# Kernel optimization log

Measured on AMD Instinct MI355X. Metric: run time of the kernel, lower is better.

Reference implementation:

```python
import jax, jax.numpy as jnp
import numpy as np

# BD feature layout (matches init_kwargs BD dict)
MARK_AX = 0
OP_SHL = 1
OP_SHR = 2
ALU_LO = 16
ALU_HI = 32
AX_CARRY_LO = 48
OUTPUT_LO = 64
OUTPUT_HI = 80
D = 128
B, S = 32, 8192


def setup_inputs() -> dict:
    key = jax.random.key(0)
    x_bd = jax.random.normal(key, (B, S, D), dtype=jnp.float32)
    return {"x_bd": x_bd}


def reference(x_bd):
    # decode operands from one-hot-ish nibble slices  [B, S]
    val_lo = jnp.argmax(x_bd[..., ALU_LO:ALU_LO + 16], axis=-1).astype(jnp.int32)
    val_hi = jnp.argmax(x_bd[..., ALU_HI:ALU_HI + 16], axis=-1).astype(jnp.int32)
    value = val_lo + (val_hi << 4)                                 # 0..255
    shift = jnp.minimum(
        jnp.argmax(x_bd[..., AX_CARRY_LO:AX_CARRY_LO + 16], axis=-1).astype(jnp.int32), 31)

    mark = x_bd[..., MARK_AX] >= 0.5
    shl = x_bd[..., OP_SHL] > 0.5
    shr = x_bd[..., OP_SHR] > 0.5
    active = mark & (shl | shr)

    pow2 = jnp.left_shift(jnp.int32(1), shift)                     # 2**shift, exact
    res_shl = (value * pow2) & 255                                 # SHL mod 256
    res_shr = value // pow2                                        # SHR floor
    result = jnp.where(shl, res_shl, res_shr)

    res_lo = result & 15
    res_hi = (result >> 4) & 15
    # scatter +2.0 into OUTPUT_LO/HI bins via one-hot (vectorized over B*S)
    add = 2.0 * (jax.nn.one_hot(OUTPUT_LO + res_lo, D, dtype=x_bd.dtype)
                 + jax.nn.one_hot(OUTPUT_HI + res_hi, D, dtype=x_bd.dtype))
    return x_bd + jnp.where(active[..., None], add, jnp.zeros((), x_bd.dtype))
```

## Files before the change

kernel.cpp:

```cpp
#include <hip/hip_runtime.h>

#define DD 128

__global__ __launch_bounds__(256) void byteshift_kernel(const float* __restrict__ x,
                                                        float* __restrict__ out,
                                                        int n_rows) {
    int tid = blockIdx.x * blockDim.x + threadIdx.x;
    int lane_r = tid & 31;
    int row = tid >> 5;
    if (row >= n_rows) return;

    const float4* xrow = (const float4*)(x + (size_t)row * DD);
    float4 v = xrow[lane_r];

    int dbase = lane_r * 4;
    float m = v.x; int mi = dbase;
    if (v.y > m) { m = v.y; mi = dbase + 1; }
    if (v.z > m) { m = v.z; mi = dbase + 2; }
    if (v.w > m) { m = v.w; mi = dbase + 3; }

    #pragma unroll
    for (int dlt = 1; dlt <= 2; dlt <<= 1) {
        float om = __shfl_xor(m, dlt);
        int   oi = __shfl_xor(mi, dlt);
        if (om > m || (om == m && oi < mi)) { m = om; mi = oi; }
    }

    int flags = (v.x >= 0.5f ? 1 : 0) | (v.y > 0.5f ? 2 : 0) | (v.z > 0.5f ? 4 : 0);
    flags = __shfl(flags, 0, 32);

    int d_lo = __shfl(mi, 4, 32);
    int d_hi = __shfl(mi, 8, 32);
    int d_sh = __shfl(mi, 12, 32);

    int value = (d_lo & 15) | ((d_hi & 15) << 4);
    int shift = d_sh & 15;
    bool shl    = (flags & 2) != 0;
    bool active = (flags & 1) && (flags & 6);
    int result = shl ? ((value << shift) & 255) : (value >> shift);
    int t0 = 64 + (result & 15);
    int t1 = 80 + ((result >> 4) & 15);

    float add = active ? 2.0f : 0.0f;
    float4 o = v;
    if (dbase     == t0 || dbase     == t1) o.x += add;
    if (dbase + 1 == t0 || dbase + 1 == t1) o.y += add;
    if (dbase + 2 == t0 || dbase + 2 == t1) o.z += add;
    if (dbase + 3 == t0 || dbase + 3 == t1) o.w += add;
    ((float4*)(out + (size_t)row * DD))[lane_r] = o;
}

extern "C" void kernel_launch(void* const* d_in, const int* in_sizes, int n_in,
                              void* d_out, int out_size, void* d_ws, size_t ws_size,
                              hipStream_t stream) {
    const float* x = (const float*)d_in[0];
    float* out = (float*)d_out;
    int n_rows = in_sizes[0] / DD;
    int threads = 256;
    int total = n_rows * 32;
    int blocks = (total + threads - 1) / threads;
    hipLaunchKernelGGL(byteshift_kernel, dim3(blocks), dim3(threads), 0, stream,
                       x, out, n_rows);
}
```

Baseline: 216.1 us.

## Map 8 lanes per row with 16 floats each and nontemporal accesses

Each thread now handles a full 16-wide nibble group (four 16-byte vectors) instead of 4 floats, so the argmax is computed in-thread with no cross-lane reduction shuffles. Rows use 8 lanes, loads and stores use nontemporal builtins, and the +2.0 scatter becomes a single per-lane index compare. This cuts shuffle and ALU work and aims for streaming memory behaviour. The trade-off is fewer threads in flight and each lane touching 64 contiguous bytes rather than the fully coalesced pattern across lanes.

```diff
diff --git a/kernel.cpp b/kernel.cpp
--- a/kernel.cpp
+++ b/kernel.cpp
@@ -1,53 +1,61 @@
 #include <hip/hip_runtime.h>
 
 #define DD 128
+
+typedef float f32x4 __attribute__((ext_vector_type(4)));
 
 __global__ __launch_bounds__(256) void byteshift_kernel(const float* __restrict__ x,
                                                         float* __restrict__ out,
                                                         int n_rows) {
     int tid = blockIdx.x * blockDim.x + threadIdx.x;
-    int lane_r = tid & 31;
-    int row = tid >> 5;
+    int lane = tid & 7;
+    int row = tid >> 3;
     if (row >= n_rows) return;
 
-    const float4* xrow = (const float4*)(x + (size_t)row * DD);
-    float4 v = xrow[lane_r];
+    const f32x4* xr = (const f32x4*)(x + (size_t)row * DD) + lane * 4;
+    f32x4 v0 = __builtin_nontemporal_load(xr + 0);
+    f32x4 v1 = __builtin_nontemporal_load(xr + 1);
+    f32x4 v2 = __builtin_nontemporal_load(xr + 2);
+    f32x4 v3 = __builtin_nontemporal_load(xr + 3);
 
-    int dbase = lane_r * 4;
-    float m = v.x; int mi = dbase;
-    if (v.y > m) { m = v.y; mi = dbase + 1; }
-    if (v.z > m) { m = v.z; mi = dbase + 2; }
-    if (v.w > m) { m = v.w; mi = dbase + 3; }
+    float f[16] = {v0.x, v0.y, v0.z, v0.w, v1.x, v1.y, v1.z, v1.w,
+                   v2.x, v2.y, v2.z, v2.w, v3.x, v3.y, v3.z, v3.w};
+
+    float m = f[0]; int mi = 0;
+    #pragma unroll
+    for (int j = 1; j < 16; ++j)
+        if (f[j] > m) { m = f[j]; mi = j; }
+
+    int flags = (f[0] >= 0.5f ? 1 : 0) | (f[1] > 0.5f ? 2 : 0) | (f[2] > 0.5f ? 4 : 0);
+    flags     = __shfl(flags, 0, 8);
+    int n_lo  = __shfl(mi, 1, 8);
+    int n_hi  = __shfl(mi, 2, 8);
+    int n_sh  = __shfl(mi, 3, 8);
+
+    int value   = n_lo | (n_hi << 4);
+    bool shl    = (flags & 2) != 0;
+    bool active = (flags & 1) && (flags & 6);
+    int result  = shl ? ((value << n_sh) & 255) : (value >> n_sh);
+
+    int t0 = 64 + (result & 15);
+    int t1 = 80 + (result >> 4);
+    int dbase = lane << 4;
+    int tsel  = (dbase == 80) ? t1 : t0;
+    int r     = active ? (tsel - dbase) : -1;
 
     #pragma unroll
-    for (int dlt = 1; dlt <= 2; dlt <<= 1) {
-        float om = __shfl_xor(m, dlt);
-        int   oi = __shfl_xor(mi, dlt);
-        if (om > m || (om == m && oi < mi)) { m = om; mi = oi; }
-    }
+    for (int j = 0; j < 16; ++j)
+        if (r == j) f[j] += 2.0f;
 
-    int flags = (v.x >= 0.5f ? 1 : 0) | (v.y > 0.5f ? 2 : 0) | (v.z > 0.5f ? 4 : 0);
-    flags = __shfl(flags, 0, 32);
-
-    int d_lo = __shfl(mi, 4, 32);
-    int d_hi = __shfl(mi, 8, 32);
-    int d_sh = __shfl(mi, 12, 32);
-
-    int value = (d_lo & 15) | ((d_hi & 15) << 4);
-    int shift = d_sh & 15;
-    bool shl    = (flags & 2) != 0;
-    bool active = (flags & 1) && (flags & 6);
-    int result = shl ? ((value << shift) & 255) : (value >> shift);
-    int t0 = 64 + (result & 15);
-    int t1 = 80 + ((result >> 4) & 15);
-
-    float add = active ? 2.0f : 0.0f;
-    float4 o = v;
-    if (dbase     == t0 || dbase     == t1) o.x += add;
-    if (dbase + 1 == t0 || dbase + 1 == t1) o.y += add;
-    if (dbase + 2 == t0 || dbase + 2 == t1) o.z += add;
-    if (dbase + 3 == t0 || dbase + 3 == t1) o.w += add;
-    ((float4*)(out + (size_t)row * DD))[lane_r] = o;
+    f32x4* orow = (f32x4*)(out + (size_t)row * DD) + lane * 4;
+    f32x4 o0 = {f[0],  f[1],  f[2],  f[3]};
+    f32x4 o1 = {f[4],  f[5],  f[6],  f[7]};
+    f32x4 o2 = {f[8],  f[9],  f[10], f[11]};
+    f32x4 o3 = {f[12], f[13], f[14], f[15]};
+    __builtin_nontemporal_store(o0, orow + 0);
+    __builtin_nontemporal_store(o1, orow + 1);
+    __builtin_nontemporal_store(o2, orow + 2);
+    __builtin_nontemporal_store(o3, orow + 3);
 }
 
 extern "C" void kernel_launch(void* const* d_in, const int* in_sizes, int n_in,
@@ -57,7 +65,7 @@
     float* out = (float*)d_out;
     int n_rows = in_sizes[0] / DD;
     int threads = 256;
-    int total = n_rows * 32;
+    int total = n_rows * 8;
     int blocks = (total + threads - 1) / threads;
     hipLaunchKernelGGL(byteshift_kernel, dim3(blocks), dim3(threads), 0, stream,
                        x, out, n_rows);
```

New measurement: 260.9 us. 20.7% more time.
